# Kernel optimization log

Measured on AMD Instinct MI355X. Metric: run time of the kernel, lower is better.

The kernel has to match this reference:

```python
import jax, jax.numpy as jnp
import numpy as np

EPS = 1e-10


def setup_inputs() -> dict:
    key = jax.random.key(0)
    ks = jax.random.split(key, 8)
    b, s, m, r, n = 2, 2048, 1024, 64, 16
    u = jax.random.normal(ks[0], (b, s, m), dtype=jnp.float32)
    delta = jax.random.normal(ks[1], (b, s, r), dtype=jnp.float32)
    dt_proj_w = jax.random.normal(ks[2], (m, r), dtype=jnp.float32) * 0.02
    dt_proj_b = jax.random.normal(ks[3], (m,), dtype=jnp.float32) * 0.02
    # A_log ~ Uniform(-3, -1) as in nn.init.uniform_(self.A_log, -3.0, -1.0)
    A_log = jax.random.uniform(ks[4], (n, m), dtype=jnp.float32, minval=-3.0, maxval=-1.0)
    D_skip = jnp.ones((m,), dtype=jnp.float32)
    # xavier_uniform with gain=0.1 on [n, m]
    bound = 0.1 * np.sqrt(6.0 / (n + m))
    B_proj_w = jax.random.uniform(ks[5], (n, m), dtype=jnp.float32, minval=-bound, maxval=bound)
    C_proj_w = jax.random.uniform(ks[6], (n, m), dtype=jnp.float32, minval=-bound, maxval=bound)
    return {"u": u, "delta": delta, "dt_proj_w": dt_proj_w, "dt_proj_b": dt_proj_b,
            "A_log": A_log, "D_skip": D_skip, "B_proj_w": B_proj_w, "C_proj_w": C_proj_w}


def reference(u, delta, dt_proj_w, dt_proj_b, A_log, D_skip, B_proj_w, C_proj_w):
    # u: [b, s, m]; delta: [b, s, r]
    dt = jax.nn.softplus(jnp.einsum('bsr,mr->bsm', delta, dt_proj_w) + dt_proj_b)
    dt = jnp.clip(dt, 1e-6, 10.0)                      # [b, s, m]
    A = jnp.clip(-jnp.exp(A_log), -10.0, -1e-6)        # [n, m]
    B = jnp.einsum('bsm,nm->bsn', u, B_proj_w)         # [b, s, n]
    C = jnp.einsum('bsm,nm->bsn', u, C_proj_w)         # [b, s, n]

    # associative-scan path (seq_len > 256), math as in _associative_scan:
    # h_t = exp(cumsum_t log(dA)) * cumsum_t (dB_u / dA)
    dA = jnp.exp(dt[:, :, None, :] * A[None, None])    # [b, s, n, m]
    dA_c = jnp.clip(dA, EPS, None)
    dBu = dt[:, :, None, :] * B[..., None] * u[:, :, None, :]  # [b, s, n, m]
    A_cum = jnp.exp(jnp.cumsum(jnp.log(dA_c), axis=1))
    h = A_cum * jnp.cumsum(dBu / dA_c, axis=1)          # [b, s, n, m]
    y = jnp.einsum('bsnm,bsn->bsm', h, C)               # contract state dim

    out = y + u * D_skip
    out = jnp.clip(out, -10000.0, 10000.0)
    bad = jnp.any(~jnp.isfinite(out))
    return jnp.where(bad, jnp.zeros_like(u), out)
```

## Files before the change

### kernel.cpp

```cpp
#include <hip/hip_runtime.h>
#include <math.h>

#define B_ 2
#define S_ 2048
#define M_ 1024
#define R_ 64
#define N_ 16
#define NC 32
#define CH 64
#define LOG2E 1.44269504088896f

#define DT_OFF  0
#define AGG_OFF 4194304
#define BWT_OFF 6291456
#define CWT_OFF 6307840
#define PB_OFF  6324224
#define PC_OFF  6455296

__global__ __launch_bounds__(256) void k_dt(const float* __restrict__ delta,
                                            const float* __restrict__ Wdt,
                                            const float* __restrict__ bdt,
                                            const float* __restrict__ Bw,
                                            const float* __restrict__ Cw,
                                            float* __restrict__ dt,
                                            float* __restrict__ BwT,
                                            float* __restrict__ CwT) {
    int bid = blockIdx.y * 4 + blockIdx.x;
    if (threadIdx.x < 8) {
        int idx = bid * 8 + threadIdx.x;
        int mt = idx >> 4, nt = idx & 15;
        BwT[idx] = Bw[nt * M_ + mt];
        CwT[idx] = Cw[nt * M_ + mt];
    }
    int m    = blockIdx.x * 256 + threadIdx.x;
    int row0 = blockIdx.y * 8;
    float w[R_];
    const float4* W4 = reinterpret_cast<const float4*>(Wdt + (size_t)m * R_);
#pragma unroll
    for (int i = 0; i < R_ / 4; ++i) {
        float4 v = W4[i];
        w[4*i] = v.x; w[4*i+1] = v.y; w[4*i+2] = v.z; w[4*i+3] = v.w;
    }
    float bias = bdt[m];
#pragma unroll 1
    for (int r = 0; r < 8; ++r) {
        int bs = row0 + r;
        const float* dr = delta + (size_t)bs * R_;
        float acc = bias;
#pragma unroll
        for (int k = 0; k < R_; ++k) acc = fmaf(dr[k], w[k], acc);
        float sp = fmaxf(acc, 0.f) + log1pf(expf(-fabsf(acc)));
        sp = fminf(fmaxf(sp, 1e-6f), 10.0f);
        dt[(size_t)bs * M_ + m] = sp;
    }
}

__global__ __launch_bounds__(256) void k_bc_partial(const float* __restrict__ u,
                                                    const float* __restrict__ BwT,
                                                    const float* __restrict__ CwT,
                                                    float* __restrict__ pB,
                                                    float* __restrict__ pC) {
    __shared__ float uLds[16 * 516];
    int r0 = blockIdx.x * 16;
    int k0 = blockIdx.y * 512;
    for (int i = threadIdx.x; i < 2048; i += 256) {
        int r = i >> 7, kq = i & 127;
        float4 v = *reinterpret_cast<const float4*>(&u[(size_t)(r0 + r) * M_ + k0 + kq * 4]);
        *reinterpret_cast<float4*>(&uLds[r * 516 + kq * 4]) = v;
    }
    __syncthreads();
    int r = threadIdx.x >> 4, n = threadIdx.x & 15;
    const float4* u4 = reinterpret_cast<const float4*>(uLds + r * 516);
    float accB = 0.f, accC = 0.f;
#pragma unroll 4
    for (int k4 = 0; k4 < 128; ++k4) {
        float4 uv = u4[k4];
        int kb = k0 + k4 * 4;
        accB = fmaf(uv.x, BwT[(kb+0)*16 + n], accB);
        accB = fmaf(uv.y, BwT[(kb+1)*16 + n], accB);
        accB = fmaf(uv.z, BwT[(kb+2)*16 + n], accB);
        accB = fmaf(uv.w, BwT[(kb+3)*16 + n], accB);
        accC = fmaf(uv.x, CwT[(kb+0)*16 + n], accC);
        accC = fmaf(uv.y, CwT[(kb+1)*16 + n], accC);
        accC = fmaf(uv.z, CwT[(kb+2)*16 + n], accC);
        accC = fmaf(uv.w, CwT[(kb+3)*16 + n], accC);
    }
    size_t o = (size_t)blockIdx.y * 65536 + (size_t)(r0 + r) * 16 + n;
    pB[o] = accB;
    pC[o] = accC;
}

__global__ __launch_bounds__(256) void k_pass1(const float* __restrict__ dt,
                                               const float* __restrict__ u,
                                               const float* __restrict__ pB,
                                               const float* __restrict__ A_log,
                                               float* __restrict__ Agg) {
    __shared__ float ldsDt[CH * 64], ldsU[CH * 64], ldsB[CH * 16];
    const int m0 = blockIdx.x * 64, c = blockIdx.y, b = blockIdx.z;
    const int s0 = c * CH;
    const int tid = threadIdx.x;
    for (int i = tid; i < 1024; i += 256) {
        int s = i >> 4, mq = (i & 15) * 4;
        size_t off = ((size_t)(b * S_ + s0 + s)) * M_ + m0 + mq;
        *reinterpret_cast<float4*>(&ldsDt[s * 64 + mq]) = *reinterpret_cast<const float4*>(&dt[off]);
        *reinterpret_cast<float4*>(&ldsU [s * 64 + mq]) = *reinterpret_cast<const float4*>(&u[off]);
    }
    {
        size_t base = (size_t)(b * S_ + s0) * N_;
        for (int i = tid; i < CH * 16; i += 256)
            ldsB[i] = pB[base + i] + pB[65536 + base + i];
    }
    __syncthreads();
    const int lane = tid & 63, wave = tid >> 6;
    const int ml = wave * 16 + (lane & 15);
    const int m  = m0 + ml;
    const int n0 = (lane >> 4) * 4;
    float Aa2[4], h[4] = {0,0,0,0}, g[4] = {1.f,1.f,1.f,1.f};
#pragma unroll
    for (int j = 0; j < 4; ++j) {
        float a = -expf(A_log[(size_t)(n0 + j) * M_ + m]);
        Aa2[j] = fminf(fmaxf(a, -10.f), -1e-6f) * LOG2E;
    }
    for (int s = 0; s < CH; ++s) {
        float dtv = ldsDt[s * 64 + ml];
        float uv  = ldsU [s * 64 + ml];
        float du  = dtv * uv;
        float4 bv = *reinterpret_cast<const float4*>(&ldsB[s * 16 + n0]);
        float bb[4] = {bv.x, bv.y, bv.z, bv.w};
#pragma unroll
        for (int j = 0; j < 4; ++j) {
            float ea = exp2f(dtv * Aa2[j]);
            h[j] = fmaf(ea, h[j], g[j] * (du * bb[j]));
            g[j] *= ea;
        }
    }
    float* dst = Agg + ((size_t)(b * 16 + blockIdx.x) * NC + c) * 2048 + tid * 8;
    *reinterpret_cast<float4*>(dst)     = make_float4(g[0], h[0], g[1], h[1]);
    *reinterpret_cast<float4*>(dst + 4) = make_float4(g[2], h[2], g[3], h[3]);
}

__global__ __launch_bounds__(256) void k_pass3(const float* __restrict__ dt,
                                               const float* __restrict__ u,
                                               const float* __restrict__ pB,
                                               const float* __restrict__ pC,
                                               const float* __restrict__ A_log,
                                               const float* __restrict__ Dskip,
                                               const float* __restrict__ Agg,
                                               float* __restrict__ out) {
    __shared__ float ldsDt[CH * 64], ldsU[CH * 64], ldsB[CH * 16], ldsC[CH * 16];
    const int m0 = blockIdx.x * 64, c = blockIdx.y, b = blockIdx.z;
    const int s0 = c * CH;
    const int tid = threadIdx.x;
    for (int i = tid; i < 1024; i += 256) {
        int s = i >> 4, mq = (i & 15) * 4;
        size_t off = ((size_t)(b * S_ + s0 + s)) * M_ + m0 + mq;
        *reinterpret_cast<float4*>(&ldsDt[s * 64 + mq]) = *reinterpret_cast<const float4*>(&dt[off]);
        *reinterpret_cast<float4*>(&ldsU [s * 64 + mq]) = *reinterpret_cast<const float4*>(&u[off]);
    }
    {
        size_t base = (size_t)(b * S_ + s0) * N_;
        for (int i = tid; i < CH * 16; i += 256) {
            ldsB[i] = pB[base + i] + pB[65536 + base + i];
            ldsC[i] = pC[base + i] + pC[65536 + base + i];
        }
    }
    const int lane = tid & 63, wave = tid >> 6;
    const int ml = wave * 16 + (lane & 15);
    const int m  = m0 + ml;
    const int ng = lane >> 4, n0 = ng * 4;

    float g[4] = {1.f,1.f,1.f,1.f}, h[4] = {0.f,0.f,0.f,0.f};
    {
        const float* aggB = Agg + (size_t)(b * 16 + blockIdx.x) * NC * 2048 + tid * 8;
        int cp = 0;
        for (; cp + 4 <= c; cp += 4) {
            float4 q[8];
#pragma unroll
            for (int t = 0; t < 4; ++t) {
                q[2*t]   = *reinterpret_cast<const float4*>(aggB + (size_t)(cp + t) * 2048);
                q[2*t+1] = *reinterpret_cast<const float4*>(aggB + (size_t)(cp + t) * 2048 + 4);
            }
#pragma unroll
            for (int t = 0; t < 4; ++t) {
                float4 a0 = q[2*t], a1 = q[2*t+1];
                h[0] = fmaf(a0.x, h[0], g[0] * a0.y); g[0] *= a0.x;
                h[1] = fmaf(a0.z, h[1], g[1] * a0.w); g[1] *= a0.z;
                h[2] = fmaf(a1.x, h[2], g[2] * a1.y); g[2] *= a1.x;
                h[3] = fmaf(a1.z, h[3], g[3] * a1.w); g[3] *= a1.z;
            }
        }
        for (; cp < c; ++cp) {
            float4 a0 = *reinterpret_cast<const float4*>(aggB + (size_t)cp * 2048);
            float4 a1 = *reinterpret_cast<const float4*>(aggB + (size_t)cp * 2048 + 4);
            h[0] = fmaf(a0.x, h[0], g[0] * a0.y); g[0] *= a0.x;
            h[1] = fmaf(a0.z, h[1], g[1] * a0.w); g[1] *= a0.z;
            h[2] = fmaf(a1.x, h[2], g[2] * a1.y); g[2] *= a1.x;
            h[3] = fmaf(a1.z, h[3], g[3] * a1.w); g[3] *= a1.z;
        }
    }
    float Aa2[4];
#pragma unroll
    for (int j = 0; j < 4; ++j) {
        float a = -expf(A_log[(size_t)(n0 + j) * M_ + m]);
        Aa2[j] = fminf(fmaxf(a, -10.f), -1e-6f) * LOG2E;
    }
    const float Dm = Dskip[m];
    __syncthreads();

    for (int s = 0; s < CH; ++s) {
        float dtv = ldsDt[s * 64 + ml];
        float uv  = ldsU [s * 64 + ml];
        float du  = dtv * uv;
        float4 bv = *reinterpret_cast<const float4*>(&ldsB[s * 16 + n0]);
        float4 cv = *reinterpret_cast<const float4*>(&ldsC[s * 16 + n0]);
        float bb[4] = {bv.x, bv.y, bv.z, bv.w};
        float cc[4] = {cv.x, cv.y, cv.z, cv.w};
        float y = 0.f;
#pragma unroll
        for (int j = 0; j < 4; ++j) {
            float ea = exp2f(dtv * Aa2[j]);
            h[j] = fmaf(ea, h[j], g[j] * (du * bb[j]));
            g[j] *= ea;
            y = fmaf(h[j], cc[j], y);
        }
        y += __shfl_xor(y, 16, 64);
        y += __shfl_xor(y, 32, 64);
        if (ng == 0) {
            float o = y + uv * Dm;
            o = fminf(fmaxf(o, -10000.f), 10000.f);
            out[((size_t)(b * S_ + s0 + s)) * M_ + m] = o;
        }
    }
}

extern "C" void kernel_launch(void* const* d_in, const int* in_sizes, int n_in,
                              void* d_out, int out_size, void* d_ws, size_t ws_size,
                              hipStream_t stream) {
    const float* u     = (const float*)d_in[0];
    const float* delta = (const float*)d_in[1];
    const float* Wdt   = (const float*)d_in[2];
    const float* bdt   = (const float*)d_in[3];
    const float* A_log = (const float*)d_in[4];
    const float* Dski  = (const float*)d_in[5];
    const float* Bw    = (const float*)d_in[6];
    const float* Cw    = (const float*)d_in[7];
    float* out = (float*)d_out;
    float* ws  = (float*)d_ws;

    float* dt  = ws + DT_OFF;
    float* Agg = ws + AGG_OFF;
    float* BwT = ws + BWT_OFF;
    float* CwT = ws + CWT_OFF;
    float* pB  = ws + PB_OFF;
    float* pC  = ws + PC_OFF;

    k_dt<<<dim3(4, 512), 256, 0, stream>>>(delta, Wdt, bdt, Bw, Cw, dt, BwT, CwT);
    k_bc_partial<<<dim3(256, 2), 256, 0, stream>>>(u, BwT, CwT, pB, pC);
    k_pass1<<<dim3(16, NC, B_), 256, 0, stream>>>(dt, u, pB, A_log, Agg);
    k_pass3<<<dim3(16, NC, B_), 256, 0, stream>>>(dt, u, pB, pC, A_log, Dski, Agg, out);
}
```

Measured before the change: 117.7 us.

## Use closed-form chunk aggregates, reduce B/C in-block, drop LDS staging in scans

k_pass1 now builds each chunk aggregate in closed form. It sums dt into T and accumulates du*B*exp(-dt*A), so the per-step g multiply chain becomes an independent accumulation plus one final exp2. k_bc now reduces both K halves inside one block with a shuffle, so the pass kernels no longer add two partial buffers. The scan kernels read dt, u, B and C directly from global memory instead of staging them in LDS, which removes the barrier. The inverse-exponential form risks overflow or precision loss for large dt*|A| within a chunk, and the direct loads are strided by M with 64-byte segments per row.

```diff
diff --git a/kernel.cpp b/kernel.cpp
--- a/kernel.cpp
+++ b/kernel.cpp
@@ -14,8 +14,8 @@
 #define AGG_OFF 4194304
 #define BWT_OFF 6291456
 #define CWT_OFF 6307840
-#define PB_OFF  6324224
-#define PC_OFF  6455296
+#define BP_OFF  6324224
+#define CP_OFF  6389760
 
 __global__ __launch_bounds__(256) void k_dt(const float* __restrict__ delta,
                                             const float* __restrict__ Wdt,
@@ -55,22 +55,25 @@
     }
 }
 
-__global__ __launch_bounds__(256) void k_bc_partial(const float* __restrict__ u,
-                                                    const float* __restrict__ BwT,
-                                                    const float* __restrict__ CwT,
-                                                    float* __restrict__ pB,
-                                                    float* __restrict__ pC) {
-    __shared__ float uLds[16 * 516];
-    int r0 = blockIdx.x * 16;
-    int k0 = blockIdx.y * 512;
-    for (int i = threadIdx.x; i < 2048; i += 256) {
-        int r = i >> 7, kq = i & 127;
-        float4 v = *reinterpret_cast<const float4*>(&u[(size_t)(r0 + r) * M_ + k0 + kq * 4]);
-        *reinterpret_cast<float4*>(&uLds[r * 516 + kq * 4]) = v;
+__global__ __launch_bounds__(256) void k_bc(const float* __restrict__ u,
+                                            const float* __restrict__ BwT,
+                                            const float* __restrict__ CwT,
+                                            float* __restrict__ Bp,
+                                            float* __restrict__ Cp) {
+    __shared__ float uLds[8 * 1032];
+    const int r0 = blockIdx.x * 8;
+    const int tid = threadIdx.x;
+    for (int i = tid; i < 2048; i += 256) {
+        int r = i >> 8, kq = i & 255;
+        *reinterpret_cast<float4*>(&uLds[r * 1032 + kq * 4]) =
+            *reinterpret_cast<const float4*>(&u[(size_t)(r0 + r) * M_ + kq * 4]);
     }
     __syncthreads();
-    int r = threadIdx.x >> 4, n = threadIdx.x & 15;
-    const float4* u4 = reinterpret_cast<const float4*>(uLds + r * 516);
+    const int r  = tid >> 5;
+    const int kh = (tid >> 4) & 1;
+    const int n  = tid & 15;
+    const int k0 = kh * 512;
+    const float4* u4 = reinterpret_cast<const float4*>(uLds + r * 1032 + k0);
     float accB = 0.f, accC = 0.f;
 #pragma unroll 4
     for (int k4 = 0; k4 < 128; ++k4) {
@@ -85,85 +88,70 @@
         accC = fmaf(uv.z, CwT[(kb+2)*16 + n], accC);
         accC = fmaf(uv.w, CwT[(kb+3)*16 + n], accC);
     }
-    size_t o = (size_t)blockIdx.y * 65536 + (size_t)(r0 + r) * 16 + n;
-    pB[o] = accB;
-    pC[o] = accC;
+    accB += __shfl_xor(accB, 16, 64);
+    accC += __shfl_xor(accC, 16, 64);
+    if (kh == 0) {
+        Bp[(size_t)(r0 + r) * N_ + n] = accB;
+        Cp[(size_t)(r0 + r) * N_ + n] = accC;
+    }
 }
 
 __global__ __launch_bounds__(256) void k_pass1(const float* __restrict__ dt,
                                                const float* __restrict__ u,
-                                               const float* __restrict__ pB,
+                                               const float* __restrict__ Bp,
                                                const float* __restrict__ A_log,
                                                float* __restrict__ Agg) {
-    __shared__ float ldsDt[CH * 64], ldsU[CH * 64], ldsB[CH * 16];
-    const int m0 = blockIdx.x * 64, c = blockIdx.y, b = blockIdx.z;
-    const int s0 = c * CH;
+    const int mt = blockIdx.x, c = blockIdx.y, b = blockIdx.z;
+    const int m0 = mt * 64, s0 = c * CH;
     const int tid = threadIdx.x;
-    for (int i = tid; i < 1024; i += 256) {
-        int s = i >> 4, mq = (i & 15) * 4;
-        size_t off = ((size_t)(b * S_ + s0 + s)) * M_ + m0 + mq;
-        *reinterpret_cast<float4*>(&ldsDt[s * 64 + mq]) = *reinterpret_cast<const float4*>(&dt[off]);
-        *reinterpret_cast<float4*>(&ldsU [s * 64 + mq]) = *reinterpret_cast<const float4*>(&u[off]);
-    }
-    {
-        size_t base = (size_t)(b * S_ + s0) * N_;
-        for (int i = tid; i < CH * 16; i += 256)
-            ldsB[i] = pB[base + i] + pB[65536 + base + i];
-    }
-    __syncthreads();
     const int lane = tid & 63, wave = tid >> 6;
     const int ml = wave * 16 + (lane & 15);
     const int m  = m0 + ml;
     const int n0 = (lane >> 4) * 4;
-    float Aa2[4], h[4] = {0,0,0,0}, g[4] = {1.f,1.f,1.f,1.f};
+    float Aa2[4];
 #pragma unroll
     for (int j = 0; j < 4; ++j) {
         float a = -expf(A_log[(size_t)(n0 + j) * M_ + m]);
         Aa2[j] = fminf(fmaxf(a, -10.f), -1e-6f) * LOG2E;
     }
+    const float*  dtp = dt + (size_t)(b * S_ + s0) * M_ + m;
+    const float*  up  = u  + (size_t)(b * S_ + s0) * M_ + m;
+    const float4* Bp4 = reinterpret_cast<const float4*>(Bp + (size_t)(b * S_ + s0) * N_) + (n0 >> 2);
+    float T = 0.f, S[4] = {0.f, 0.f, 0.f, 0.f};
+#pragma unroll 2
     for (int s = 0; s < CH; ++s) {
-        float dtv = ldsDt[s * 64 + ml];
-        float uv  = ldsU [s * 64 + ml];
+        float dtv = dtp[(size_t)s * M_];
+        float uv  = up [(size_t)s * M_];
+        float4 bv = Bp4[s * 4];
         float du  = dtv * uv;
-        float4 bv = *reinterpret_cast<const float4*>(&ldsB[s * 16 + n0]);
-        float bb[4] = {bv.x, bv.y, bv.z, bv.w};
-#pragma unroll
-        for (int j = 0; j < 4; ++j) {
-            float ea = exp2f(dtv * Aa2[j]);
-            h[j] = fmaf(ea, h[j], g[j] * (du * bb[j]));
-            g[j] *= ea;
-        }
-    }
-    float* dst = Agg + ((size_t)(b * 16 + blockIdx.x) * NC + c) * 2048 + tid * 8;
+        T += dtv;
+        S[0] = fmaf(du * bv.x, exp2f(-dtv * Aa2[0]), S[0]);
+        S[1] = fmaf(du * bv.y, exp2f(-dtv * Aa2[1]), S[1]);
+        S[2] = fmaf(du * bv.z, exp2f(-dtv * Aa2[2]), S[2]);
+        S[3] = fmaf(du * bv.w, exp2f(-dtv * Aa2[3]), S[3]);
+    }
+    float g[4], h[4];
+#pragma unroll
+    for (int j = 0; j < 4; ++j) {
+        g[j] = exp2f(Aa2[j] * T);
+        h[j] = g[j] * S[j];
+    }
+    float* dst = Agg + ((size_t)(b * 16 + mt) * NC + c) * 2048 + tid * 8;
     *reinterpret_cast<float4*>(dst)     = make_float4(g[0], h[0], g[1], h[1]);
     *reinterpret_cast<float4*>(dst + 4) = make_float4(g[2], h[2], g[3], h[3]);
 }
 
 __global__ __launch_bounds__(256) void k_pass3(const float* __restrict__ dt,
                                                const float* __restrict__ u,
-                                               const float* __restrict__ pB,
-                                               const float* __restrict__ pC,
+                                               const float* __restrict__ Bp,
+                                               const float* __restrict__ Cp,
                                                const float* __restrict__ A_log,
                                                const float* __restrict__ Dskip,
                                                const float* __restrict__ Agg,
                                                float* __restrict__ out) {
-    __shared__ float ldsDt[CH * 64], ldsU[CH * 64], ldsB[CH * 16], ldsC[CH * 16];
-    const int m0 = blockIdx.x * 64, c = blockIdx.y, b = blockIdx.z;
-    const int s0 = c * CH;
+    const int mt = blockIdx.x, c = blockIdx.y, b = blockIdx.z;
+    const int m0 = mt * 64, s0 = c * CH;
     const int tid = threadIdx.x;
-    for (int i = tid; i < 1024; i += 256) {
-        int s = i >> 4, mq = (i & 15) * 4;
-        size_t off = ((size_t)(b * S_ + s0 + s)) * M_ + m0 + mq;
-        *reinterpret_cast<float4*>(&ldsDt[s * 64 + mq]) = *reinterpret_cast<const float4*>(&dt[off]);
-        *reinterpret_cast<float4*>(&ldsU [s * 64 + mq]) = *reinterpret_cast<const float4*>(&u[off]);
-    }
-    {
-        size_t base = (size_t)(b * S_ + s0) * N_;
-        for (int i = tid; i < CH * 16; i += 256) {
-            ldsB[i] = pB[base + i] + pB[65536 + base + i];
-            ldsC[i] = pC[base + i] + pC[65536 + base + i];
-        }
-    }
     const int lane = tid & 63, wave = tid >> 6;
     const int ml = wave * 16 + (lane & 15);
     const int m  = m0 + ml;
@@ -171,7 +159,7 @@
 
     float g[4] = {1.f,1.f,1.f,1.f}, h[4] = {0.f,0.f,0.f,0.f};
     {
-        const float* aggB = Agg + (size_t)(b * 16 + blockIdx.x) * NC * 2048 + tid * 8;
+        const float* aggB = Agg + (size_t)(b * 16 + mt) * NC * 2048 + tid * 8;
         int cp = 0;
         for (; cp + 4 <= c; cp += 4) {
             float4 q[8];
@@ -205,14 +193,19 @@
         Aa2[j] = fminf(fmaxf(a, -10.f), -1e-6f) * LOG2E;
     }
     const float Dm = Dskip[m];
-    __syncthreads();
-
+    const float*  dtp = dt + (size_t)(b * S_ + s0) * M_ + m;
+    const float*  up  = u  + (size_t)(b * S_ + s0) * M_ + m;
+    const float4* Bp4 = reinterpret_cast<const float4*>(Bp + (size_t)(b * S_ + s0) * N_) + (n0 >> 2);
+    const float4* Cp4 = reinterpret_cast<const float4*>(Cp + (size_t)(b * S_ + s0) * N_) + (n0 >> 2);
+    float* outp = out + (size_t)(b * S_ + s0) * M_ + m;
+
+#pragma unroll 2
     for (int s = 0; s < CH; ++s) {
-        float dtv = ldsDt[s * 64 + ml];
-        float uv  = ldsU [s * 64 + ml];
+        float dtv = dtp[(size_t)s * M_];
+        float uv  = up [(size_t)s * M_];
+        float4 bv = Bp4[s * 4];
+        float4 cv = Cp4[s * 4];
         float du  = dtv * uv;
-        float4 bv = *reinterpret_cast<const float4*>(&ldsB[s * 16 + n0]);
-        float4 cv = *reinterpret_cast<const float4*>(&ldsC[s * 16 + n0]);
         float bb[4] = {bv.x, bv.y, bv.z, bv.w};
         float cc[4] = {cv.x, cv.y, cv.z, cv.w};
         float y = 0.f;
@@ -228,7 +221,7 @@
         if (ng == 0) {
             float o = y + uv * Dm;
             o = fminf(fmaxf(o, -10000.f), 10000.f);
-            out[((size_t)(b * S_ + s0 + s)) * M_ + m] = o;
+            outp[(size_t)s * M_] = o;
         }
     }
 }
@@ -251,11 +244,11 @@
     float* Agg = ws + AGG_OFF;
     float* BwT = ws + BWT_OFF;
     float* CwT = ws + CWT_OFF;
-    float* pB  = ws + PB_OFF;
-    float* pC  = ws + PC_OFF;
+    float* Bp  = ws + BP_OFF;
+    float* Cp  = ws + CP_OFF;
 
     k_dt<<<dim3(4, 512), 256, 0, stream>>>(delta, Wdt, bdt, Bw, Cw, dt, BwT, CwT);
-    k_bc_partial<<<dim3(256, 2), 256, 0, stream>>>(u, BwT, CwT, pB, pC);
-    k_pass1<<<dim3(16, NC, B_), 256, 0, stream>>>(dt, u, pB, A_log, Agg);
-    k_pass3<<<dim3(16, NC, B_), 256, 0, stream>>>(dt, u, pB, pC, A_log, Dski, Agg, out);
-}
+    k_bc<<<512, 256, 0, stream>>>(u, BwT, CwT, Bp, Cp);
+    k_pass1<<<dim3(16, NC, B_), 256, 0, stream>>>(dt, u, Bp, A_log, Agg);
+    k_pass3<<<dim3(16, NC, B_), 256, 0, stream>>>(dt, u, Bp, Cp, A_log, Dski, Agg, out);
+}
```

Measured after the change: 122.6 us. 4.1% more time.
